# Kernel optimization log

Hardware: AMD Instinct MI355X
Metric: run time of the kernel (lower is better)

## Reference

```python
import jax, jax.numpy as jnp
import numpy as np

ALPHA = 0.5   # leak rate
GAMMA = 0.01  # input scaling
RHO = 1.0     # target spectral radius
SPARSITY = 0.9  # fraction of zeros in W

T, N_INPUT, N_OUTPUT = 4096, 8192, 2048


def setup_inputs() -> dict:
    key = jax.random.key(0)
    k1, k2, k3, k4 = jax.random.split(key, 4)
    x = jax.random.normal(k1, (T, N_INPUT), dtype=jnp.float32)
    Win = GAMMA * jax.random.normal(k2, (N_INPUT, N_OUTPUT), dtype=jnp.float32)
    mask = (jax.random.uniform(k3, (N_OUTPUT, N_OUTPUT)) < (1.0 - SPARSITY)).astype(jnp.float32)
    W0 = jax.random.normal(k4, (N_OUTPUT, N_OUTPUT), dtype=jnp.float32) * mask
    # spectral-radius normalization (circular-law estimate: radius ~ sqrt(p * N) for
    # density p), standing in for rho * W / max|eig(W)| at init time.
    W = RHO * W0 / jnp.sqrt((1.0 - SPARSITY) * N_OUTPUT)
    return {"x": x, "W": W, "Win": Win}


def reference(x, W, Win):
    # x: [T, nInput]; output: [T, nOutput] (stacked hidden states)
    u_proj = x @ Win  # [T, nOutput], input projection is independent of the recurrence

    def step(v, up):
        # v: [nOutput]  leaky-integrator reservoir update
        v_new = (1.0 - ALPHA) * v + ALPHA * jnp.tanh(v @ W + up)
        return v_new, v_new

    v0 = jnp.zeros((W.shape[0],), dtype=x.dtype)  # ESN starts from zero state
    _, vs = jax.lax.scan(step, v0, u_proj)
    return vs
```

## Files before the change

### kernel.cpp

```cpp
#include <hip/hip_runtime.h>
#include <hip/hip_bf16.h>
#include <math.h>

#define T_STEPS 4096
#define N_IN    8192
#define N_OUT   2048

#define RB    64
#define CPB   32
#define GRP   8
#define CAP   288
#define KMAX  (CAP / GRP)
#define NMT   32
#define GEMM_BLOCKS 512
#define GM_BK 32

#define SM_ENT   0
#define SM_CNTS  73728
#define SM_VSH   (73728 + 128)
#define SM_BYTES (73728 + 128 + 16384)
#define SM_GA    0
#define SM_GB    16896

__device__ __forceinline__ float fast_tanh(float x) {
    const float ax = fabsf(x);
    const float e  = __expf(2.0f * ax);
    const float r  = __builtin_amdgcn_rcpf(e + 1.0f);
    const float t  = 1.0f - 2.0f * r;
    return copysignf(t, x);
}

__global__ __launch_bounds__(256, 1) void esn_fused(
        const float* __restrict__ X,
        const float* __restrict__ W,
        const float* __restrict__ Win,
        float* __restrict__ UO,
        unsigned long long* vslots,
        int* mcnt) {
    __shared__ __align__(16) char smem[SM_BYTES];
    const int tid = threadIdx.x;

    if (blockIdx.x >= RB) {
        float (*As)[132] = reinterpret_cast<float(*)[132]>(smem + SM_GA);
        float (*Bs)[132] = reinterpret_cast<float(*)[132]>(smem + SM_GB);
        const int gb = (int)blockIdx.x - RB;
        const int bm = gb >> 4;
        const int bn = gb & 15;
        const int K = N_IN, N = N_OUT;
        const int tx = tid & 15;
        const int ty = tid >> 4;

        float acc[8][8];
#pragma unroll
        for (int i = 0; i < 8; i++)
#pragma unroll
            for (int jj = 0; jj < 8; jj++) acc[i][jj] = 0.f;

        const float* Xb = X + (size_t)(bm * 128) * K;
        const float* Wb = Win + bn * 128;

        for (int kt = 0; kt < K; kt += GM_BK) {
#pragma unroll
            for (int q = 0; q < 4; q++) {
                const int r  = (tid >> 3) + q * 32;
                const int c4 = (tid & 7) * 4;
                const float4 a4 = *reinterpret_cast<const float4*>(&Xb[(size_t)r * K + kt + c4]);
                As[c4 + 0][r] = a4.x;
                As[c4 + 1][r] = a4.y;
                As[c4 + 2][r] = a4.z;
                As[c4 + 3][r] = a4.w;
            }
#pragma unroll
            for (int q = 0; q < 4; q++) {
                const int r  = (tid >> 5) + q * 8;
                const int c4 = (tid & 31) * 4;
                *reinterpret_cast<float4*>(&Bs[r][c4]) =
                    *reinterpret_cast<const float4*>(&Wb[(size_t)(kt + r) * N + c4]);
            }
            __syncthreads();

#pragma unroll
            for (int k = 0; k < GM_BK; k++) {
                float a[8], bb[8];
#pragma unroll
                for (int i = 0; i < 4; i++) {
                    a[i]     = As[k][ty * 4 + i];
                    a[4 + i] = As[k][64 + ty * 4 + i];
                }
#pragma unroll
                for (int jj = 0; jj < 4; jj++) {
                    bb[jj]     = Bs[k][tx * 4 + jj];
                    bb[4 + jj] = Bs[k][64 + tx * 4 + jj];
                }
#pragma unroll
                for (int i = 0; i < 8; i++)
#pragma unroll
                    for (int jj = 0; jj < 8; jj++)
                        acc[i][jj] = fmaf(a[i], bb[jj], acc[i][jj]);
            }
            __syncthreads();
        }

#pragma unroll
        for (int i = 0; i < 8; i++) {
            const int mr = bm * 128 + ((i < 4) ? (ty * 4 + i) : (64 + ty * 4 + (i - 4)));
            float* Crow = UO + (size_t)mr * N + bn * 128;
            float4 v0 = make_float4(acc[i][0], acc[i][1], acc[i][2], acc[i][3]);
            float4 v1 = make_float4(acc[i][4], acc[i][5], acc[i][6], acc[i][7]);
            *reinterpret_cast<float4*>(&Crow[tx * 4])      = v0;
            *reinterpret_cast<float4*>(&Crow[64 + tx * 4]) = v1;
        }
        __syncthreads();
        if (tid == 0)
            __hip_atomic_fetch_add(&mcnt[bm], 1, __ATOMIC_RELEASE,
                                   __HIP_MEMORY_SCOPE_AGENT);
        return;
    }

    __builtin_amdgcn_s_setprio(1);
    auto ent  = reinterpret_cast<unsigned long long(*)[CAP]>(smem + SM_ENT);
    int* cnts = reinterpret_cast<int*>(smem + SM_CNTS);
    float (*vsh)[N_OUT] = reinterpret_cast<float(*)[N_OUT]>(smem + SM_VSH);

    const int b   = blockIdx.x;
    const int c   = tid >> 3;
    const int l   = tid & 7;
    const int j   = b * CPB + c;
    const int lw  = tid & 63;

    int cnt = 0;
    for (int k = 0; k < N_OUT / GRP; k++) {
        const float w = W[(size_t)(l + GRP * k) * N_OUT + j];
        cnt += (w != 0.0f) ? 1 : 0;
    }
    int inc = cnt;
#pragma unroll
    for (int d = 1; d < GRP; d <<= 1) {
        int n = __shfl_up(inc, d, 64);
        if (l >= d) inc += n;
    }
    int pos = inc - cnt;
    if (l == GRP - 1) cnts[c] = inc;
    for (int k = 0; k < N_OUT / GRP; k++) {
        const int i = l + GRP * k;
        const float w = W[(size_t)i * N_OUT + j];
        if (w != 0.0f) {
            if (pos < CAP)
                ent[c][pos] = ((unsigned long long)(unsigned)i << 32) | __float_as_uint(w);
            pos++;
        }
    }
    __syncthreads();
    const int ccnt = min(cnts[c], CAP);

    float wreg[KMAX];
    int   ireg[KMAX];
#pragma unroll
    for (int k = 0; k < KMAX; k++) {
        const int p = l + k * GRP;
        if (p < ccnt) {
            const unsigned long long e = ent[c][p];
            wreg[k] = __uint_as_float((unsigned)e);
            ireg[k] = (int)(e >> 32);
        } else {
            wreg[k] = 0.f;
            ireg[k] = 0;
        }
    }

#pragma unroll
    for (int pass = 0; pass < KMAX; ++pass) {
#pragma unroll
        for (int i = (pass & 1); i + 1 < KMAX; i += 2) {
            const int ka = ((ireg[i]     & 31) - lw) & 31;
            const int kb = ((ireg[i + 1] & 31) - lw) & 31;
            const bool sw = ka > kb;
            const int   ti = sw ? ireg[i] : ireg[i + 1];
            const int   bi = sw ? ireg[i + 1] : ireg[i];
            const float tw = sw ? wreg[i] : wreg[i + 1];
            const float bw = sw ? wreg[i + 1] : wreg[i];
            ireg[i] = bi; ireg[i + 1] = ti;
            wreg[i] = bw; wreg[i + 1] = tw;
        }
    }

    float vold = 0.f;

#pragma unroll 1
    for (int t = 0; t < T_STEPS; t++) {
        if ((t & 127) == 0) {
            while (__hip_atomic_load(&mcnt[t >> 7], __ATOMIC_ACQUIRE,
                                     __HIP_MEMORY_SCOPE_AGENT) < 16) { }
        }
        float u = 0.f;
        if (l == 0) u = UO[(size_t)t * N_OUT + j];

        unsigned long long* vin = vslots + (size_t)(t & 1) * N_OUT;
        float* dst = vsh[t & 1];
        unsigned long long uq[8];
#pragma unroll
        for (int q = 0; q < 8; q++)
            uq[q] = __hip_atomic_load(&vin[tid + q * 256], __ATOMIC_RELAXED,
                                      __HIP_MEMORY_SCOPE_AGENT);
        unsigned pend = 0xFFu;
#pragma unroll 1
        while (true) {
            unsigned np = 0;
#pragma unroll
            for (int q = 0; q < 8; q++) {
                if (pend & (1u << q)) {
                    if ((unsigned)(uq[q] >> 32) == (unsigned)t)
                        dst[tid + q * 256] = __uint_as_float((unsigned)uq[q]);
                    else
                        np |= (1u << q);
                }
            }
            pend = np;
            if (!pend) break;
#pragma unroll
            for (int q = 0; q < 8; q++)
                if (pend & (1u << q))
                    uq[q] = __hip_atomic_load(&vin[tid + q * 256], __ATOMIC_RELAXED,
                                              __HIP_MEMORY_SCOPE_AGENT);
        }
        __syncthreads();

        const float* vcur = vsh[t & 1];
        float y0 = 0.f, y1 = 0.f, y2 = 0.f, y3 = 0.f;
#pragma unroll
        for (int k = 0; k < KMAX; k += 4) {
            y0 = fmaf(wreg[k + 0], vcur[ireg[k + 0]], y0);
            y1 = fmaf(wreg[k + 1], vcur[ireg[k + 1]], y1);
            y2 = fmaf(wreg[k + 2], vcur[ireg[k + 2]], y2);
            y3 = fmaf(wreg[k + 3], vcur[ireg[k + 3]], y3);
        }
        float y = (y0 + y1) + (y2 + y3);
#pragma unroll
        for (int d = GRP / 2; d >= 1; d >>= 1) y += __shfl_xor(y, d, 64);

        if (l == 0) {
            const float vnew = 0.5f * vold + 0.5f * fast_tanh(y + u);
            vold = vnew;
            const unsigned long long slot =
                ((unsigned long long)(unsigned)(t + 1) << 32) | __float_as_uint(vnew);
            __hip_atomic_store(&vslots[(size_t)((t + 1) & 1) * N_OUT + j], slot,
                               __ATOMIC_RELAXED, __HIP_MEMORY_SCOPE_AGENT);
            UO[(size_t)t * N_OUT + j] = vnew;
        }
    }
}

extern "C" void kernel_launch(void* const* d_in, const int* in_sizes, int n_in,
                              void* d_out, int out_size, void* d_ws, size_t ws_size,
                              hipStream_t stream) {
    const float* x   = (const float*)d_in[0];
    const float* W   = (const float*)d_in[1];
    const float* Win = (const float*)d_in[2];
    float* out = (float*)d_out;

    unsigned long long* vslots = (unsigned long long*)d_ws;
    int* mcnt = (int*)((char*)d_ws + 2 * N_OUT * sizeof(unsigned long long));

    hipMemsetAsync(d_ws, 0,
                   2 * N_OUT * sizeof(unsigned long long) + NMT * sizeof(int),
                   stream);

    esn_fused<<<RB + GEMM_BLOCKS, 256, 0, stream>>>(x, W, Win, out, vslots, mcnt);
}
```

Baseline: 11.17 ms.

## Shrink GEMM grid to persistent tiles and skip empty sparse MAC slots

```diff
diff --git a/kernel.cpp b/kernel.cpp
--- a/kernel.cpp
+++ b/kernel.cpp
@@ -12,7 +12,7 @@
 #define CAP   288
 #define KMAX  (CAP / GRP)
 #define NMT   32
-#define GEMM_BLOCKS 512
+#define GEMM_BLOCKS 128
 #define GM_BK 32
 
 #define SM_ENT   0
@@ -44,76 +44,82 @@
         float (*As)[132] = reinterpret_cast<float(*)[132]>(smem + SM_GA);
         float (*Bs)[132] = reinterpret_cast<float(*)[132]>(smem + SM_GB);
         const int gb = (int)blockIdx.x - RB;
-        const int bm = gb >> 4;
-        const int bn = gb & 15;
         const int K = N_IN, N = N_OUT;
         const int tx = tid & 15;
         const int ty = tid >> 4;
 
-        float acc[8][8];
-#pragma unroll
-        for (int i = 0; i < 8; i++)
-#pragma unroll
-            for (int jj = 0; jj < 8; jj++) acc[i][jj] = 0.f;
-
-        const float* Xb = X + (size_t)(bm * 128) * K;
-        const float* Wb = Win + bn * 128;
-
-        for (int kt = 0; kt < K; kt += GM_BK) {
-#pragma unroll
-            for (int q = 0; q < 4; q++) {
-                const int r  = (tid >> 3) + q * 32;
-                const int c4 = (tid & 7) * 4;
-                const float4 a4 = *reinterpret_cast<const float4*>(&Xb[(size_t)r * K + kt + c4]);
-                As[c4 + 0][r] = a4.x;
-                As[c4 + 1][r] = a4.y;
-                As[c4 + 2][r] = a4.z;
-                As[c4 + 3][r] = a4.w;
+#pragma unroll 1
+        for (int s = 0; s < 4; ++s) {
+            const int tile = gb + 128 * s;
+            const int bm = tile >> 4;
+            const int bn = tile & 15;
+
+            float acc[8][8];
+#pragma unroll
+            for (int i = 0; i < 8; i++)
+#pragma unroll
+                for (int jj = 0; jj < 8; jj++) acc[i][jj] = 0.f;
+
+            const float* Xb = X + (size_t)(bm * 128) * K;
+            const float* Wb = Win + bn * 128;
+
+            for (int kt = 0; kt < K; kt += GM_BK) {
+#pragma unroll
+                for (int q = 0; q < 4; q++) {
+                    const int r  = (tid >> 3) + q * 32;
+                    const int c4 = (tid & 7) * 4;
+                    const float4 a4 = *reinterpret_cast<const float4*>(&Xb[(size_t)r * K + kt + c4]);
+                    As[c4 + 0][r] = a4.x;
+                    As[c4 + 1][r] = a4.y;
+                    As[c4 + 2][r] = a4.z;
+                    As[c4 + 3][r] = a4.w;
+                }
+#pragma unroll
+                for (int q = 0; q < 4; q++) {
+                    const int r  = (tid >> 5) + q * 8;
+                    const int c4 = (tid & 31) * 4;
+                    *reinterpret_cast<float4*>(&Bs[r][c4]) =
+                        *reinterpret_cast<const float4*>(&Wb[(size_t)(kt + r) * N + c4]);
+                }
+                __syncthreads();
+
+#pragma unroll
+                for (int k = 0; k < GM_BK; k++) {
+                    float a[8], bb[8];
+#pragma unroll
+                    for (int i = 0; i < 4; i++) {
+                        a[i]     = As[k][ty * 4 + i];
+                        a[4 + i] = As[k][64 + ty * 4 + i];
+                    }
+#pragma unroll
+                    for (int jj = 0; jj < 4; jj++) {
+                        bb[jj]     = Bs[k][tx * 4 + jj];
+                        bb[4 + jj] = Bs[k][64 + tx * 4 + jj];
+                    }
+#pragma unroll
+                    for (int i = 0; i < 8; i++)
+#pragma unroll
+                        for (int jj = 0; jj < 8; jj++)
+                            acc[i][jj] = fmaf(a[i], bb[jj], acc[i][jj]);
+                }
+                __syncthreads();
             }
-#pragma unroll
-            for (int q = 0; q < 4; q++) {
-                const int r  = (tid >> 5) + q * 8;
-                const int c4 = (tid & 31) * 4;
-                *reinterpret_cast<float4*>(&Bs[r][c4]) =
-                    *reinterpret_cast<const float4*>(&Wb[(size_t)(kt + r) * N + c4]);
+
+#pragma unroll
+            for (int i = 0; i < 8; i++) {
+                const int mr = bm * 128 + ((i < 4) ? (ty * 4 + i) : (64 + ty * 4 + (i - 4)));
+                float* Crow = UO + (size_t)mr * N + bn * 128;
+                float4 v0 = make_float4(acc[i][0], acc[i][1], acc[i][2], acc[i][3]);
+                float4 v1 = make_float4(acc[i][4], acc[i][5], acc[i][6], acc[i][7]);
+                *reinterpret_cast<float4*>(&Crow[tx * 4])      = v0;
+                *reinterpret_cast<float4*>(&Crow[64 + tx * 4]) = v1;
             }
             __syncthreads();
-
-#pragma unroll
-            for (int k = 0; k < GM_BK; k++) {
-                float a[8], bb[8];
-#pragma unroll
-                for (int i = 0; i < 4; i++) {
-                    a[i]     = As[k][ty * 4 + i];
-                    a[4 + i] = As[k][64 + ty * 4 + i];
-                }
-#pragma unroll
-                for (int jj = 0; jj < 4; jj++) {
-                    bb[jj]     = Bs[k][tx * 4 + jj];
-                    bb[4 + jj] = Bs[k][64 + tx * 4 + jj];
-                }
-#pragma unroll
-                for (int i = 0; i < 8; i++)
-#pragma unroll
-                    for (int jj = 0; jj < 8; jj++)
-                        acc[i][jj] = fmaf(a[i], bb[jj], acc[i][jj]);
-            }
+            if (tid == 0)
+                __hip_atomic_fetch_add(&mcnt[bm], 1, __ATOMIC_RELEASE,
+                                       __HIP_MEMORY_SCOPE_AGENT);
             __syncthreads();
         }
-
-#pragma unroll
-        for (int i = 0; i < 8; i++) {
-            const int mr = bm * 128 + ((i < 4) ? (ty * 4 + i) : (64 + ty * 4 + (i - 4)));
-            float* Crow = UO + (size_t)mr * N + bn * 128;
-            float4 v0 = make_float4(acc[i][0], acc[i][1], acc[i][2], acc[i][3]);
-            float4 v1 = make_float4(acc[i][4], acc[i][5], acc[i][6], acc[i][7]);
-            *reinterpret_cast<float4*>(&Crow[tx * 4])      = v0;
-            *reinterpret_cast<float4*>(&Crow[64 + tx * 4]) = v1;
-        }
-        __syncthreads();
-        if (tid == 0)
-            __hip_atomic_fetch_add(&mcnt[bm], 1, __ATOMIC_RELEASE,
-                                   __HIP_MEMORY_SCOPE_AGENT);
         return;
     }
 
@@ -168,12 +174,20 @@
         }
     }
 
+    int kmw = (ccnt + GRP - 1) >> 3;
+#pragma unroll
+    for (int d = 1; d < 64; d <<= 1) {
+        const int o = __shfl_xor(kmw, d, 64);
+        kmw = (o > kmw) ? o : kmw;
+    }
+    if (kmw > KMAX) kmw = KMAX;
+
 #pragma unroll
     for (int pass = 0; pass < KMAX; ++pass) {
 #pragma unroll
         for (int i = (pass & 1); i + 1 < KMAX; i += 2) {
-            const int ka = ((ireg[i]     & 31) - lw) & 31;
-            const int kb = ((ireg[i + 1] & 31) - lw) & 31;
+            const int ka = (wreg[i]     == 0.f) ? 64 : (((ireg[i]     & 31) - lw) & 31);
+            const int kb = (wreg[i + 1] == 0.f) ? 64 : (((ireg[i + 1] & 31) - lw) & 31);
             const bool sw = ka > kb;
             const int   ti = sw ? ireg[i] : ireg[i + 1];
             const int   bi = sw ? ireg[i + 1] : ireg[i];
@@ -226,15 +240,18 @@
         __syncthreads();
 
         const float* vcur = vsh[t & 1];
-        float y0 = 0.f, y1 = 0.f, y2 = 0.f, y3 = 0.f;
-#pragma unroll
-        for (int k = 0; k < KMAX; k += 4) {
-            y0 = fmaf(wreg[k + 0], vcur[ireg[k + 0]], y0);
-            y1 = fmaf(wreg[k + 1], vcur[ireg[k + 1]], y1);
-            y2 = fmaf(wreg[k + 2], vcur[ireg[k + 2]], y2);
-            y3 = fmaf(wreg[k + 3], vcur[ireg[k + 3]], y3);
-        }
-        float y = (y0 + y1) + (y2 + y3);
+        float yy[4] = {0.f, 0.f, 0.f, 0.f};
+#define MACK(k) yy[(k) & 3] = fmaf(wreg[(k)], vcur[ireg[(k)]], yy[(k) & 3])
+#pragma unroll
+        for (int k = 0; k < 20; k += 4) {
+            MACK(k + 0); MACK(k + 1); MACK(k + 2); MACK(k + 3);
+        }
+        if (kmw > 20) { MACK(20); MACK(21); MACK(22); MACK(23); }
+        if (kmw > 24) { MACK(24); MACK(25); MACK(26); MACK(27); }
+        if (kmw > 28) { MACK(28); MACK(29); MACK(30); MACK(31); }
+        if (kmw > 32) { MACK(32); MACK(33); MACK(34); MACK(35); }
+#undef MACK
+        float y = (yy[0] + yy[1]) + (yy[2] + yy[3]);
 #pragma unroll
         for (int d = GRP / 2; d >= 1; d >>= 1) y += __shfl_xor(y, d, 64);
 
```

Result: slower. 11.72 ms (+4.9%).
